# Kernel tuning notes

Hardware: AMD Instinct MI355X
Metric: run time of the kernel (lower is better)

The kernel has to match this reference:

```python
import jax, jax.numpy as jnp
import numpy as np

B, T, D, M, L = 4, 2048, 256, 128, 16
P = M * L  # max_pair_cnt


def setup_inputs() -> dict:
    key = jax.random.key(0)
    ks = jax.random.split(key, 11)
    head = jax.random.normal(ks[0], (B, P, T), jnp.float32) * 0.05
    tail = jax.random.normal(ks[1], (B, P, T), jnp.float32) * 0.05
    x = jax.random.normal(ks[2], (B, T, D), jnp.float32)
    coref_mention_position = jax.random.uniform(ks[3], (B, M, T), jnp.float32)
    lab = jax.random.uniform(ks[4], (B, P, 2), jnp.float32) + 1e-3
    coref_label = lab / lab.sum(-1, keepdims=True)  # already-softmaxed target
    coref_label_mask = jax.random.randint(ks[5], (B, P), 0, 2).astype(bool)
    lens = jnp.full((B, M), L, jnp.int32)  # uniform segment lengths
    w1 = jax.random.normal(ks[6], (3 * D, D), jnp.float32) / np.sqrt(3 * D).astype(np.float32)
    b1 = jnp.zeros((D,), jnp.float32)
    w2 = jax.random.normal(ks[7], (D, 2), jnp.float32) / np.sqrt(D).astype(np.float32)
    b2 = jnp.zeros((2,), jnp.float32)
    return {"head": head, "tail": tail, "lens": lens, "x": x,
            "coref_mention_position": coref_mention_position,
            "coref_label": coref_label, "coref_label_mask": coref_label_mask,
            "w1": w1, "b1": b1, "w2": w2, "b2": b2}


def reference(head, tail, lens, x, coref_mention_position, coref_label,
              coref_label_mask, w1, b1, w2, b2):
    # bmm-based gather of mention reps: [B,P,T] @ [B,T,D] -> [B,P,D]
    head_rep = jnp.einsum('bpt,btd->bpd', head, x)
    tail_rep = jnp.einsum('bpt,btd->bpd', tail, x)
    feat = jnp.concatenate([head_rep, tail_rep, head_rep * tail_rep], axis=-1)
    logits = jax.nn.relu(feat @ w1 + b1) @ w2 + b2  # [B,P,2]

    # ragged split_n_pad -> per-mention top-1 select (uniform lens == L -> reshape)
    scores = logits[..., 1].reshape(B, M, L)            # [B,M,L]
    max_idx = jnp.argmax(scores, axis=-1)               # [B,M]
    max_val = jnp.max(scores, axis=-1)                  # [B,M] (raw logit, as in source)
    tail_seg = tail_rep.reshape(B, M, L, D)
    sel = jnp.take_along_axis(tail_seg, max_idx[:, :, None, None], axis=2)[:, :, 0, :]
    coref_rep_m = sel * max_val[:, :, None]             # [B,M,D]

    # scatter-bmm merge back into sequence: [B,T,M] @ [B,M,D] -> [B,T,D]
    coref_rep = jnp.einsum('bmt,bmd->btd', coref_mention_position, coref_rep_m)
    output = x + coref_rep

    # KLDivLoss(reduction='mean') over masked pairs
    logq = jax.nn.log_softmax(logits, axis=-1)
    lab = coref_label
    pw = jnp.where(lab > 0, lab * jnp.log(jnp.maximum(lab, 1e-38)), 0.0) - lab * logq
    n = jnp.sum(coref_label_mask).astype(jnp.float32)
    loss = jnp.where(coref_label_mask[..., None], pw, 0.0).sum() / (n * 2.0)
    return output, loss
```

## Files before the change

kernel.cpp:

```cpp
#include <hip/hip_runtime.h>
#include <hip/hip_bf16.h>
#include <stdint.h>

#define TAU 0.35f

typedef __attribute__((ext_vector_type(8))) short bf16x8;
typedef __attribute__((ext_vector_type(4))) float f32x4;

__device__ __forceinline__ unsigned short f2bf(float f) {
  __bf16 h = (__bf16)f;
  return __builtin_bit_cast(unsigned short, h);
}
__device__ __forceinline__ float bf2f(unsigned short u) {
  unsigned int v = ((unsigned int)u) << 16;
  return __builtin_bit_cast(float, v);
}
__device__ __forceinline__ void async_copy16(const void* g, void* l) {
  __builtin_amdgcn_global_load_lds(
      (const __attribute__((address_space(1))) unsigned int*)g,
      (__attribute__((address_space(3))) unsigned int*)l, 16, 0, 0);
}
__device__ __forceinline__ float rdlane(float v, int l) {
  return __builtin_bit_cast(float,
      __builtin_amdgcn_readlane(__builtin_bit_cast(int, v), l));
}

__global__ __launch_bounds__(256) void k_prep(
    const float* __restrict__ x, const float* __restrict__ w1,
    const float* __restrict__ b2,
    unsigned short* __restrict__ xt, unsigned short* __restrict__ w1t,
    float* __restrict__ logits, int* __restrict__ njobs,
    float* __restrict__ featws) {
  __shared__ float tileS[64][65];
  __shared__ float tx[64][132];
  int bx = blockIdx.x, tid = threadIdx.x;
  if (bx == 0 && tid < 4) njobs[tid] = 0;
  if (bx < 64) {
    int i = bx * 256 + tid;
    logits[i] = b2[i & 1];
  }
  {
    float4 z = {0.f, 0.f, 0.f, 0.f};
    for (int i = bx * 256 + tid; i < 1048576; i += 304 * 256)
      ((float4*)featws)[i] = z;
  }
  if (bx < 256) {
    int b = bx >> 6, kc = (bx >> 1) & 31, dh = bx & 1;
    const float* src = x + ((size_t)b * 2048 + (size_t)kc * 64) * 256 + dh * 128;
#pragma unroll
    for (int p = 0; p < 8; ++p) {
      int idx = p * 256 + tid;
      int row = idx >> 5, f4 = idx & 31;
      *(float4*)&tx[row][f4 * 4] = *(const float4*)&src[(size_t)row * 256 + f4 * 4];
    }
    __syncthreads();
    unsigned short* dst = xt + ((size_t)(b * 32 + kc)) * 16384 + dh * 1024;
#pragma unroll
    for (int p = 0; p < 4; ++p) {
      int idx = p * 256 + tid;
      int d0 = idx & 127, k8 = idx >> 7;
      bf16x8 v;
#pragma unroll
      for (int j = 0; j < 8; ++j) v[j] = (short)f2bf(tx[k8 * 8 + j][d0]);
      *(bf16x8*)&dst[(size_t)k8 * 2048 + d0 * 8] = v;
    }
  } else {
    int wt = bx - 256;
    int k6 = wt >> 2, n6 = wt & 3;
    int j = tid & 63, i0 = tid >> 6;
    const float* src = w1 + ((size_t)k6 * 64) * 256 + n6 * 64;
    for (int i = i0; i < 64; i += 4) tileS[i][j] = src[(size_t)i * 256 + j];
    __syncthreads();
    unsigned short* dst = w1t + ((size_t)n6 * 64) * 768 + k6 * 64;
    for (int r = i0; r < 64; r += 4) dst[(size_t)r * 768 + j] = f2bf(tileS[j][r]);
  }
}

__global__ __launch_bounds__(512, 4) void k_gemm_rep(
    const float* __restrict__ head, const float* __restrict__ tail,
    const unsigned short* __restrict__ xt,
    float* __restrict__ hrep, float* __restrict__ trep) {
  __shared__ unsigned short As[2][2048];
  __shared__ unsigned short Bs[2][16384];
  int bx = blockIdx.x;
  int b = bx >> 7, mt = bx & 127;
  const float* Asrc = ((mt < 64) ? head : tail) +
                      ((size_t)(b * 2048 + (mt & 63) * 32)) * 2048;
  float* Crep = (mt < 64) ? hrep : trep;
  const unsigned short* Bsrc = xt + (size_t)b * 524288;

  int tid = threadIdx.x, lane = tid & 63, w = tid >> 6;
  int rg = w & 1, cg = w >> 1;
  int l4 = lane >> 4, l15 = lane & 15;

  int arow = tid >> 3, ak8 = tid & 7;
  const float* aptr = Asrc + (size_t)arow * 2048 + ak8 * 8;
  int awi = (ak8 * 32 + arow) * 8;

  const unsigned short* bg = Bsrc + tid * 8;

  int aoff[2];
  int boff[2][4];
#pragma unroll
  for (int kh = 0; kh < 2; ++kh) {
    aoff[kh] = ((kh * 4 + l4) * 32 + rg * 16 + l15) * 8;
#pragma unroll
    for (int ct = 0; ct < 4; ++ct)
      boff[kh][ct] = ((kh * 4 + l4) * 256 + cg * 64 + ct * 16 + l15) * 8;
  }

  f32x4 acc[4];
#pragma unroll
  for (int ct = 0; ct < 4; ++ct) acc[ct] = (f32x4){0.f, 0.f, 0.f, 0.f};

  float4 av0, av1;
  auto STAGEB = [&](int buf) {
#pragma unroll
    for (int a = 0; a < 4; ++a)
      async_copy16(bg + (size_t)a * 4096, &Bs[buf][(tid + a * 512) * 8]);
    bg += 16384;
  };
  auto LOADA = [&]() {
    const float4* ap = (const float4*)aptr;
    av0 = ap[0]; av1 = ap[1];
    aptr += 64;
  };
  auto WRITEA = [&](int buf) {
    bf16x8 p;
    p[0] = (short)f2bf(av0.x); p[1] = (short)f2bf(av0.y);
    p[2] = (short)f2bf(av0.z); p[3] = (short)f2bf(av0.w);
    p[4] = (short)f2bf(av1.x); p[5] = (short)f2bf(av1.y);
    p[6] = (short)f2bf(av1.z); p[7] = (short)f2bf(av1.w);
    *(bf16x8*)&As[buf][awi] = p;
  };
  auto MMA = [&](int buf) {
    const unsigned short* A_ = As[buf];
    const unsigned short* B_ = Bs[buf];
#pragma unroll
    for (int kh = 0; kh < 2; ++kh) {
      bf16x8 a0 = *(const bf16x8*)&A_[aoff[kh]];
#pragma unroll
      for (int ct = 0; ct < 4; ++ct) {
        bf16x8 bb = *(const bf16x8*)&B_[boff[kh][ct]];
        acc[ct] = __builtin_amdgcn_mfma_f32_16x16x32_bf16(a0, bb, acc[ct], 0, 0, 0);
      }
    }
  };

  STAGEB(0);
  if (tid < 256) { LOADA(); WRITEA(0); }
  __syncthreads();

  for (int it = 0; it < 32; ++it) {
    int cur = it & 1, nxt = cur ^ 1;
    if (it < 31) {
      STAGEB(nxt);
      if (tid < 256) LOADA();
    }
    MMA(cur);
    if (it < 31 && tid < 256) WRITEA(nxt);
    __syncthreads();
  }

  size_t prow = (size_t)b * 2048 + (size_t)(mt & 63) * 32 + rg * 16 + (l4 << 2);
  int cb = cg * 64 + l15;
#pragma unroll
  for (int ct = 0; ct < 4; ++ct)
#pragma unroll
    for (int i = 0; i < 4; ++i)
      Crep[(prow + i) * 256 + cb + ct * 16] = acc[ct][i];
}

__global__ __launch_bounds__(256) void k_feat(
    const float* __restrict__ hrep, const float* __restrict__ trep,
    unsigned short* __restrict__ featbf) {
  int gid = blockIdx.x * 256 + threadIdx.x;
  int p = gid >> 6, d0 = (gid & 63) * 4;
  float4 h4 = *(const float4*)&hrep[(size_t)p * 256 + d0];
  float4 t4 = *(const float4*)&trep[(size_t)p * 256 + d0];
  ushort4 a, bb, c;
  a.x = f2bf(h4.x); a.y = f2bf(h4.y); a.z = f2bf(h4.z); a.w = f2bf(h4.w);
  bb.x = f2bf(t4.x); bb.y = f2bf(t4.y); bb.z = f2bf(t4.z); bb.w = f2bf(t4.w);
  c.x = f2bf(h4.x * t4.x); c.y = f2bf(h4.y * t4.y);
  c.z = f2bf(h4.z * t4.z); c.w = f2bf(h4.w * t4.w);
  *(ushort4*)&featbf[(size_t)p * 768 + d0] = a;
  *(ushort4*)&featbf[(size_t)p * 768 + 256 + d0] = bb;
  *(ushort4*)&featbf[(size_t)p * 768 + 512 + d0] = c;
}

__global__ __launch_bounds__(256, 4) void k_gemm_mlp(
    const unsigned short* __restrict__ featb, const unsigned short* __restrict__ w1t,
    const float* __restrict__ b1, const float* __restrict__ w2,
    float* __restrict__ logits) {
  __shared__ unsigned short As[2][4096], Bs[2][4096];
  int bx = blockIdx.x;
  int ntile = bx >> 7;
  int mtile = bx & 127;
  int tid = threadIdx.x, lane = tid & 63, w = tid >> 6;

  const unsigned short* ag[2];
  const unsigned short* bgp[2];
  int dofs[2];
#pragma unroll
  for (int a = 0; a < 2; ++a) {
    int rowofs = a * 8 + (lane >> 3);
    int k8 = (lane & 7) ^ (rowofs & 7);
    ag[a] = featb + (size_t)(mtile * 64 + w * 16 + rowofs) * 768 + k8 * 8;
    bgp[a] = w1t + (size_t)(ntile * 64 + w * 16 + rowofs) * 768 + k8 * 8;
    dofs[a] = (w * 128 + a * 64 + lane) * 8;
  }
  int sw0 = (lane >> 4) ^ (lane & 7);
  int sw1 = (4 + (lane >> 4)) ^ (lane & 7);
  int arowc = (w * 16 + (lane & 15)) * 8;
  int colc[4];
#pragma unroll
  for (int ct = 0; ct < 4; ++ct) colc[ct] = (ct * 16 + (lane & 15)) * 8;

  f32x4 acc[4];
#pragma unroll
  for (int ct = 0; ct < 4; ++ct) acc[ct] = (f32x4){0.f, 0.f, 0.f, 0.f};

#pragma unroll
  for (int a = 0; a < 2; ++a) {
    async_copy16(ag[a], &As[0][dofs[a]]); ag[a] += 64;
    async_copy16(bgp[a], &Bs[0][dofs[a]]); bgp[a] += 64;
  }
  __syncthreads();

  for (int it = 0; it < 12; ++it) {
    int cur = it & 1, nxt = cur ^ 1;
    if (it < 11) {
#pragma unroll
      for (int a = 0; a < 2; ++a) {
        async_copy16(ag[a], &As[nxt][dofs[a]]); ag[a] += 64;
        async_copy16(bgp[a], &Bs[nxt][dofs[a]]); bgp[a] += 64;
      }
    }
    const unsigned short* A_ = As[cur];
    const unsigned short* B_ = Bs[cur];
    bf16x8 a0 = *(const bf16x8*)&A_[(arowc + sw0) * 8];
    bf16x8 a1 = *(const bf16x8*)&A_[(arowc + sw1) * 8];
#pragma unroll
    for (int ct = 0; ct < 4; ++ct) {
      bf16x8 b0 = *(const bf16x8*)&B_[(colc[ct] + sw0) * 8];
      acc[ct] = __builtin_amdgcn_mfma_f32_16x16x32_bf16(a0, b0, acc[ct], 0, 0, 0);
    }
#pragma unroll
    for (int ct = 0; ct < 4; ++ct) {
      bf16x8 b1 = *(const bf16x8*)&B_[(colc[ct] + sw1) * 8];
      acc[ct] = __builtin_amdgcn_mfma_f32_16x16x32_bf16(a1, b1, acc[ct], 0, 0, 0);
    }
    __syncthreads();
  }

  float bv[4], w20[4], w21[4];
#pragma unroll
  for (int ct = 0; ct < 4; ++ct) {
    int col = ntile * 64 + ct * 16 + (lane & 15);
    bv[ct] = b1[col]; w20[ct] = w2[col * 2]; w21[ct] = w2[col * 2 + 1];
  }
#pragma unroll
  for (int i = 0; i < 4; ++i) {
    float s0 = 0.f, s1 = 0.f;
#pragma unroll
    for (int ct = 0; ct < 4; ++ct) {
      float r = fmaxf(acc[ct][i] + bv[ct], 0.f);
      s0 += r * w20[ct]; s1 += r * w21[ct];
    }
#pragma unroll
    for (int off = 1; off < 16; off <<= 1) {
      s0 += __shfl_xor(s0, off); s1 += __shfl_xor(s1, off);
    }
    if ((lane & 15) == 0) {
      int row = mtile * 64 + w * 16 + ((lane >> 4) << 2) + i;
      atomicAdd(&logits[row * 2], s0);
      atomicAdd(&logits[row * 2 + 1], s1);
    }
  }
}

__global__ void k_select(const float* __restrict__ logits, int* __restrict__ idxv,
                         float* __restrict__ mval, int* __restrict__ cmask,
                         int* __restrict__ njobs, int* __restrict__ jobs) {
  int q = blockIdx.x * 256 + threadIdx.x;
  if (q >= 512) return;
  int base = q * 16;
  float s[16];
#pragma unroll
  for (int i = 0; i < 16; ++i) s[i] = logits[(size_t)(base + i) * 2 + 1];
  float best = s[0]; int bi = 0;
#pragma unroll
  for (int i = 1; i < 16; ++i) if (s[i] > best) { best = s[i]; bi = i; }
  int mask = 0, cnt = 0;
#pragma unroll
  for (int i = 0; i < 16; ++i) if (s[i] > best - TAU) { mask |= 1 << i; ++cnt; }
  idxv[q] = bi; mval[q] = best;
  if (cnt > 1) {
    cmask[q] = mask;
    int bb = q >> 7;
    for (int i = 0; i < 16; ++i)
      if ((mask >> i) & 1) {
        int j = atomicAdd(&njobs[bb], 1);
        jobs[bb * 2048 + j] = base + i;
      }
  } else cmask[q] = 0;
}

__global__ __launch_bounds__(1024) void k_refine_dot(
    const int* __restrict__ njobs, const int* __restrict__ jobs,
    const float* __restrict__ head, const float* __restrict__ tail,
    const float* __restrict__ x,
    float* __restrict__ featH, float* __restrict__ featT) {
  __shared__ float red[4][16][256];
  __shared__ int scode[8];
  int tid = threadIdx.x, lane = tid & 63, w = tid >> 6;
  int tg = w >> 2, dg = w & 3;
  int d = dg * 64 + lane;

  for (int gt = blockIdx.x; ; gt += gridDim.x) {
    int rem = gt, b = 0, nj = 0;
    for (; b < 4; ++b) {
      nj = njobs[b];
      int ntb = ((nj + 7) >> 3) * 8;
      if (rem < ntb) break;
      rem -= ntb;
    }
    if (b == 4) break;
    int grp = rem >> 3, tc = rem & 7;
    __syncthreads();
    if (tid < 8) scode[tid] = jobs[b * 2048 + min(grp * 8 + tid, nj - 1)];
    __syncthreads();

    int t0 = tc * 256 + tg * 64;
    float vh[8], vt[8];
#pragma unroll
    for (int j = 0; j < 8; ++j) {
      int p = scode[j] & 2047;
      size_t ro = ((size_t)(b * 2048 + p)) * 2048 + t0 + lane;
      vh[j] = head[ro]; vt[j] = tail[ro];
    }
    float ah[8] = {0.f, 0.f, 0.f, 0.f, 0.f, 0.f, 0.f, 0.f};
    float at[8] = {0.f, 0.f, 0.f, 0.f, 0.f, 0.f, 0.f, 0.f};
    const float* xp = x + (size_t)b * 524288 + (size_t)t0 * 256 + d;
#pragma unroll 8
    for (int t = 0; t < 64; ++t) {
      float xv = xp[(size_t)t * 256];
#pragma unroll
      for (int j = 0; j < 8; ++j) {
        ah[j] += rdlane(vh[j], t) * xv;
        at[j] += rdlane(vt[j], t) * xv;
      }
    }
#pragma unroll
    for (int j = 0; j < 8; ++j) {
      red[tg][j][d] = ah[j];
      red[tg][8 + j][d] = at[j];
    }
    __syncthreads();
    if (tid < 256) {
#pragma unroll
      for (int j = 0; j < 16; ++j) {
        float s = red[0][j][tid] + red[1][j][tid] + red[2][j][tid] + red[3][j][tid];
        int jj = j & 7;
        if (grp * 8 + jj < nj) {
          float* dst = (j < 8) ? featH : featT;
          atomicAdd(&dst[(size_t)scode[jj] * 256 + tid], s);
        }
      }
    }
  }
}

__global__ __launch_bounds__(1024) void k_refine_mlp(
    const int* __restrict__ njobs, const int* __restrict__ jobs,
    const float* __restrict__ featH, const float* __restrict__ featT,
    const float* __restrict__ w1, const float* __restrict__ b1,
    const float* __restrict__ w2, const float* __restrict__ b2,
    float* __restrict__ refined) {
  __shared__ float feat8[768][8];
  __shared__ float redm[4][8][256];
  __shared__ float part[8][4];
  __shared__ int scode[8];
  int tid = threadIdx.x;
  int hseg = tid >> 8, d = tid & 255;

  for (int gt = blockIdx.x; ; gt += gridDim.x) {
    int rem = gt, b = 0, nj = 0;
    for (; b < 4; ++b) {
      nj = njobs[b];
      int ntb = (nj + 7) >> 3;
      if (rem < ntb) break;
      rem -= ntb;
    }
    if (b == 4) break;
    int grp = rem;
    __syncthreads();
    if (tid < 8) scode[tid] = jobs[b * 2048 + min(grp * 8 + tid, nj - 1)];
    __syncthreads();
#pragma unroll
    for (int r = 0; r < 2; ++r) {
      int j = hseg * 2 + r;
      float h = featH[(size_t)scode[j] * 256 + d];
      float t = featT[(size_t)scode[j] * 256 + d];
      feat8[d][j] = h; feat8[256 + d][j] = t; feat8[512 + d][j] = h * t;
    }
    __syncthreads();
    float hp[8] = {0.f, 0.f, 0.f, 0.f, 0.f, 0.f, 0.f, 0.f};
    const float* w1c = w1 + (size_t)(hseg * 192) * 256 + d;
#pragma unroll 4
    for (int ii = 0; ii < 192; ++ii) {
      float wv = w1c[(size_t)ii * 256];
      float4 f0 = *(const float4*)&feat8[hseg * 192 + ii][0];
      float4 f1 = *(const float4*)&feat8[hseg * 192 + ii][4];
      hp[0] += f0.x * wv; hp[1] += f0.y * wv; hp[2] += f0.z * wv; hp[3] += f0.w * wv;
      hp[4] += f1.x * wv; hp[5] += f1.y * wv; hp[6] += f1.z * wv; hp[7] += f1.w * wv;
    }
#pragma unroll
    for (int j = 0; j < 8; ++j) redm[hseg][j][d] = hp[j];
    __syncthreads();
    if (tid < 256) {
      float w2v = w2[tid * 2 + 1], b1v = b1[tid];
#pragma unroll
      for (int j = 0; j < 8; ++j) {
        float h = b1v + redm[0][j][tid] + redm[1][j][tid] + redm[2][j][tid] + redm[3][j][tid];
        h = fmaxf(h, 0.f) * w2v;
#pragma unroll
        for (int off = 1; off < 64; off <<= 1) h += __shfl_xor(h, off);
        if ((tid & 63) == 0) part[j][tid >> 6] = h;
      }
    }
    __syncthreads();
    if (tid < 8 && grp * 8 + tid < nj)
      refined[scode[tid]] = part[tid][0] + part[tid][1] + part[tid][2] + part[tid][3] + b2[1];
  }
}

__global__ __launch_bounds__(256) void k_repm(
    const int* __restrict__ idxv, const float* __restrict__ mval,
    const int* __restrict__ cmask, const float* __restrict__ refined,
    const float* __restrict__ trep, float* __restrict__ repm) {
  int q = blockIdx.x, d = threadIdx.x;
  int mask = cmask[q]; int bi; float v;
  if (mask) {
    bi = -1; v = -1e30f;
    for (int i = 0; i < 16; ++i)
      if ((mask >> i) & 1) { float s = refined[q * 16 + i]; if (s > v) { v = s; bi = i; } }
  } else { bi = idxv[q]; v = mval[q]; }
  repm[(size_t)q * 256 + d] = trep[((size_t)q * 16 + bi) * 256 + d] * v;
}

__global__ __launch_bounds__(256) void k_merge(
    const float* __restrict__ cmp, const float* __restrict__ repm,
    const float* __restrict__ x, float* __restrict__ out) {
  __shared__ float cl[128 * 16];
  int bx = blockIdx.x, b = bx >> 7, t0 = (bx & 127) * 16;
  int tid = threadIdx.x;
#pragma unroll
  for (int it = 0; it < 2; ++it) {
    int f = it * 256 + tid;
    int row = f >> 2, c4 = (f & 3) * 4;
    *(float4*)&cl[row * 16 + c4] =
        *(const float4*)&cmp[((size_t)(b * 128 + row)) * 2048 + t0 + c4];
  }
  __syncthreads();
  float acc[16];
#pragma unroll
  for (int i = 0; i < 16; ++i) acc[i] = 0.f;
  int d = tid;
  for (int m = 0; m < 128; ++m) {
    float rv = repm[(size_t)(b * 128 + m) * 256 + d];
    const float4* c4p = (const float4*)&cl[m * 16];
#pragma unroll
    for (int jj = 0; jj < 4; ++jj) {
      float4 c = c4p[jj];
      acc[jj * 4] += c.x * rv; acc[jj * 4 + 1] += c.y * rv;
      acc[jj * 4 + 2] += c.z * rv; acc[jj * 4 + 3] += c.w * rv;
    }
  }
  const float* xb = x + ((size_t)(b * 2048 + t0)) * 256 + d;
  float* ob = out + ((size_t)(b * 2048 + t0)) * 256 + d;
#pragma unroll
  for (int tt = 0; tt < 16; ++tt) ob[(size_t)tt * 256] = xb[(size_t)tt * 256] + acc[tt];
}

__global__ __launch_bounds__(1024) void k_loss(
    const float* __restrict__ logits, const float* __restrict__ lab,
    const unsigned char* __restrict__ mask, float* __restrict__ out_loss) {
  __shared__ float rs[1024], rc[1024];
  int tid = threadIdx.x;
  float sum = 0.f, cnt = 0.f;
  for (int p = tid; p < 8192; p += 1024) {
    float l0 = logits[(size_t)p * 2], l1 = logits[(size_t)p * 2 + 1];
    float a0 = lab[(size_t)p * 2], a1 = lab[(size_t)p * 2 + 1];
    float mx = fmaxf(l0, l1);
    float lse = mx + logf(expf(l0 - mx) + expf(l1 - mx));
    float pw = 0.f;
    if (a0 > 0.f) pw += a0 * logf(fmaxf(a0, 1e-38f));
    if (a1 > 0.f) pw += a1 * logf(fmaxf(a1, 1e-38f));
    pw -= a0 * (l0 - lse) + a1 * (l1 - lse);
    if (mask[p]) { sum += pw; cnt += 1.f; }
  }
  rs[tid] = sum; rc[tid] = cnt;
  __syncthreads();
  for (int s = 512; s > 0; s >>= 1) {
    if (tid < s) { rs[tid] += rs[tid + s]; rc[tid] += rc[tid + s]; }
    __syncthreads();
  }
  if (tid == 0) *out_loss = rs[0] / (rc[0] * 2.0f);
}

extern "C" void kernel_launch(void* const* d_in, const int* in_sizes, int n_in,
                              void* d_out, int out_size, void* d_ws, size_t ws_size,
                              hipStream_t stream) {
  (void)in_sizes; (void)n_in; (void)out_size; (void)ws_size;
  const float* head = (const float*)d_in[0];
  const float* tail = (const float*)d_in[1];
  const float* x = (const float*)d_in[3];
  const float* cmp = (const float*)d_in[4];
  const float* lab = (const float*)d_in[5];
  const unsigned char* lmask = (const unsigned char*)d_in[6];
  const float* w1 = (const float*)d_in[7];
  const float* b1 = (const float*)d_in[8];
  const float* w2 = (const float*)d_in[9];
  const float* b2 = (const float*)d_in[10];
  float* out = (float*)d_out;

  char* ws = (char*)d_ws;
  size_t off = 0;
  auto alloc = [&](size_t bytes) -> void* {
    void* p = ws + off; off += (bytes + 255) & ~(size_t)255; return p;
  };
  unsigned short* xt = (unsigned short*)alloc(4ull * 256 * 2048 * 2);
  unsigned short* w1t = (unsigned short*)alloc(256ull * 768 * 2);
  float* hrep = (float*)alloc(8192ull * 256 * 4);
  float* trep = (float*)alloc(8192ull * 256 * 4);
  unsigned short* featb = (unsigned short*)alloc(8192ull * 768 * 2);
  float* logits = (float*)alloc(8192ull * 2 * 4);
  float* refined = (float*)alloc(8192ull * 4);
  int* idxv = (int*)alloc(512 * 4);
  float* mvalv = (float*)alloc(512 * 4);
  int* cmaskv = (int*)alloc(512 * 4);
  int* njobs = (int*)alloc(256);
  int* jobs = (int*)alloc(4 * 2048 * 4);
  float* repm = (float*)alloc(512ull * 256 * 4);
  float* featH = (float*)alloc(8192ull * 256 * 4);
  float* featT = (float*)alloc(8192ull * 256 * 4);

  k_prep<<<304, 256, 0, stream>>>(x, w1, b2, xt, w1t, logits, njobs, featH);
  k_gemm_rep<<<512, 512, 0, stream>>>(head, tail, xt, hrep, trep);
  k_feat<<<2048, 256, 0, stream>>>(hrep, trep, featb);
  k_gemm_mlp<<<512, 256, 0, stream>>>(featb, w1t, b1, w2, logits);
  k_select<<<2, 256, 0, stream>>>(logits, idxv, mvalv, cmaskv, njobs, jobs);
  k_refine_dot<<<512, 1024, 0, stream>>>(njobs, jobs, head, tail, x, featH, featT);
  k_refine_mlp<<<128, 1024, 0, stream>>>(njobs, jobs, featH, featT, w1, b1, w2, b2, refined);
  k_repm<<<512, 256, 0, stream>>>(idxv, mvalv, cmaskv, refined, trep, repm);
  k_merge<<<512, 256, 0, stream>>>(cmp, repm, x, out);
  k_loss<<<1, 1024, 0, stream>>>(logits, lab, lmask, out + 4ull * 2048 * 256);
}
```

Measured before the change: 320.8 us.

## Halve K-step in rep GEMM to cut LDS and fuse select with loss

The head/tail representation GEMM now stages 32-wide K slices instead of 64, halving its LDS footprint. This lets more blocks sit on each CU, and the launch bound is raised to 8 to match, at the cost of twice as many loop iterations and barriers. The top-1 select and the KL loss reduction are merged into a single 512-thread kernel to remove one tiny launch from the tail of the pipeline.

Result: slower. 344.2 us (+7.3%).

```diff
diff --git a/kernel.cpp b/kernel.cpp
--- a/kernel.cpp
+++ b/kernel.cpp
@@ -76,12 +76,12 @@
   }
 }
 
-__global__ __launch_bounds__(512, 4) void k_gemm_rep(
+__global__ __launch_bounds__(512, 8) void k_gemm_rep(
     const float* __restrict__ head, const float* __restrict__ tail,
     const unsigned short* __restrict__ xt,
     float* __restrict__ hrep, float* __restrict__ trep) {
-  __shared__ unsigned short As[2][2048];
-  __shared__ unsigned short Bs[2][16384];
+  __shared__ unsigned short As[2][1024];
+  __shared__ unsigned short Bs[2][8192];
   int bx = blockIdx.x;
   int b = bx >> 7, mt = bx & 127;
   const float* Asrc = ((mt < 64) ? head : tail) +
@@ -93,21 +93,17 @@
   int rg = w & 1, cg = w >> 1;
   int l4 = lane >> 4, l15 = lane & 15;
 
-  int arow = tid >> 3, ak8 = tid & 7;
+  int arow = tid >> 2, ak8 = tid & 3;
   const float* aptr = Asrc + (size_t)arow * 2048 + ak8 * 8;
   int awi = (ak8 * 32 + arow) * 8;
 
   const unsigned short* bg = Bsrc + tid * 8;
 
-  int aoff[2];
-  int boff[2][4];
-#pragma unroll
-  for (int kh = 0; kh < 2; ++kh) {
-    aoff[kh] = ((kh * 4 + l4) * 32 + rg * 16 + l15) * 8;
-#pragma unroll
-    for (int ct = 0; ct < 4; ++ct)
-      boff[kh][ct] = ((kh * 4 + l4) * 256 + cg * 64 + ct * 16 + l15) * 8;
-  }
+  int aoff = (l4 * 32 + rg * 16 + l15) * 8;
+  int boff[4];
+#pragma unroll
+  for (int ct = 0; ct < 4; ++ct)
+    boff[ct] = (l4 * 256 + cg * 64 + ct * 16 + l15) * 8;
 
   f32x4 acc[4];
 #pragma unroll
@@ -116,14 +112,14 @@
   float4 av0, av1;
   auto STAGEB = [&](int buf) {
 #pragma unroll
-    for (int a = 0; a < 4; ++a)
+    for (int a = 0; a < 2; ++a)
       async_copy16(bg + (size_t)a * 4096, &Bs[buf][(tid + a * 512) * 8]);
-    bg += 16384;
+    bg += 8192;
   };
   auto LOADA = [&]() {
     const float4* ap = (const float4*)aptr;
     av0 = ap[0]; av1 = ap[1];
-    aptr += 64;
+    aptr += 32;
   };
   auto WRITEA = [&](int buf) {
     bf16x8 p;
@@ -136,29 +132,26 @@
   auto MMA = [&](int buf) {
     const unsigned short* A_ = As[buf];
     const unsigned short* B_ = Bs[buf];
-#pragma unroll
-    for (int kh = 0; kh < 2; ++kh) {
-      bf16x8 a0 = *(const bf16x8*)&A_[aoff[kh]];
-#pragma unroll
-      for (int ct = 0; ct < 4; ++ct) {
-        bf16x8 bb = *(const bf16x8*)&B_[boff[kh][ct]];
-        acc[ct] = __builtin_amdgcn_mfma_f32_16x16x32_bf16(a0, bb, acc[ct], 0, 0, 0);
-      }
+    bf16x8 a0 = *(const bf16x8*)&A_[aoff];
+#pragma unroll
+    for (int ct = 0; ct < 4; ++ct) {
+      bf16x8 bb = *(const bf16x8*)&B_[boff[ct]];
+      acc[ct] = __builtin_amdgcn_mfma_f32_16x16x32_bf16(a0, bb, acc[ct], 0, 0, 0);
     }
   };
 
   STAGEB(0);
-  if (tid < 256) { LOADA(); WRITEA(0); }
+  if (tid < 128) { LOADA(); WRITEA(0); }
   __syncthreads();
 
-  for (int it = 0; it < 32; ++it) {
+  for (int it = 0; it < 64; ++it) {
     int cur = it & 1, nxt = cur ^ 1;
-    if (it < 31) {
+    if (it < 63) {
       STAGEB(nxt);
-      if (tid < 256) LOADA();
+      if (tid < 128) LOADA();
     }
     MMA(cur);
-    if (it < 31 && tid < 256) WRITEA(nxt);
+    if (it < 63 && tid < 128) WRITEA(nxt);
     __syncthreads();
   }
 
@@ -279,31 +272,56 @@
   }
 }
 
-__global__ void k_select(const float* __restrict__ logits, int* __restrict__ idxv,
-                         float* __restrict__ mval, int* __restrict__ cmask,
-                         int* __restrict__ njobs, int* __restrict__ jobs) {
-  int q = blockIdx.x * 256 + threadIdx.x;
-  if (q >= 512) return;
-  int base = q * 16;
-  float s[16];
-#pragma unroll
-  for (int i = 0; i < 16; ++i) s[i] = logits[(size_t)(base + i) * 2 + 1];
-  float best = s[0]; int bi = 0;
-#pragma unroll
-  for (int i = 1; i < 16; ++i) if (s[i] > best) { best = s[i]; bi = i; }
-  int mask = 0, cnt = 0;
-#pragma unroll
-  for (int i = 0; i < 16; ++i) if (s[i] > best - TAU) { mask |= 1 << i; ++cnt; }
-  idxv[q] = bi; mval[q] = best;
-  if (cnt > 1) {
-    cmask[q] = mask;
-    int bb = q >> 7;
-    for (int i = 0; i < 16; ++i)
-      if ((mask >> i) & 1) {
-        int j = atomicAdd(&njobs[bb], 1);
-        jobs[bb * 2048 + j] = base + i;
-      }
-  } else cmask[q] = 0;
+__global__ __launch_bounds__(512) void k_select_loss(
+    const float* __restrict__ logits, int* __restrict__ idxv,
+    float* __restrict__ mval, int* __restrict__ cmask,
+    int* __restrict__ njobs, int* __restrict__ jobs,
+    const float* __restrict__ lab, const unsigned char* __restrict__ mask,
+    float* __restrict__ out_loss) {
+  __shared__ float rs[512], rc[512];
+  int tid = threadIdx.x;
+  {
+    int q = tid;
+    int base = q * 16;
+    float s[16];
+#pragma unroll
+    for (int i = 0; i < 16; ++i) s[i] = logits[(size_t)(base + i) * 2 + 1];
+    float best = s[0]; int bi = 0;
+#pragma unroll
+    for (int i = 1; i < 16; ++i) if (s[i] > best) { best = s[i]; bi = i; }
+    int msk = 0, cnt = 0;
+#pragma unroll
+    for (int i = 0; i < 16; ++i) if (s[i] > best - TAU) { msk |= 1 << i; ++cnt; }
+    idxv[q] = bi; mval[q] = best;
+    if (cnt > 1) {
+      cmask[q] = msk;
+      int bb = q >> 7;
+      for (int i = 0; i < 16; ++i)
+        if ((msk >> i) & 1) {
+          int j = atomicAdd(&njobs[bb], 1);
+          jobs[bb * 2048 + j] = base + i;
+        }
+    } else cmask[q] = 0;
+  }
+  float sum = 0.f, cnt = 0.f;
+  for (int p = tid; p < 8192; p += 512) {
+    float l0 = logits[(size_t)p * 2], l1 = logits[(size_t)p * 2 + 1];
+    float a0 = lab[(size_t)p * 2], a1 = lab[(size_t)p * 2 + 1];
+    float mx = fmaxf(l0, l1);
+    float lse = mx + logf(expf(l0 - mx) + expf(l1 - mx));
+    float pw = 0.f;
+    if (a0 > 0.f) pw += a0 * logf(fmaxf(a0, 1e-38f));
+    if (a1 > 0.f) pw += a1 * logf(fmaxf(a1, 1e-38f));
+    pw -= a0 * (l0 - lse) + a1 * (l1 - lse);
+    if (mask[p]) { sum += pw; cnt += 1.f; }
+  }
+  rs[tid] = sum; rc[tid] = cnt;
+  __syncthreads();
+  for (int s = 256; s > 0; s >>= 1) {
+    if (tid < s) { rs[tid] += rs[tid + s]; rc[tid] += rc[tid + s]; }
+    __syncthreads();
+  }
+  if (tid == 0) *out_loss = rs[0] / (rc[0] * 2.0f);
 }
 
 __global__ __launch_bounds__(1024) void k_refine_dot(
@@ -481,32 +499,6 @@
   float* ob = out + ((size_t)(b * 2048 + t0)) * 256 + d;
 #pragma unroll
   for (int tt = 0; tt < 16; ++tt) ob[(size_t)tt * 256] = xb[(size_t)tt * 256] + acc[tt];
-}
-
-__global__ __launch_bounds__(1024) void k_loss(
-    const float* __restrict__ logits, const float* __restrict__ lab,
-    const unsigned char* __restrict__ mask, float* __restrict__ out_loss) {
-  __shared__ float rs[1024], rc[1024];
-  int tid = threadIdx.x;
-  float sum = 0.f, cnt = 0.f;
-  for (int p = tid; p < 8192; p += 1024) {
-    float l0 = logits[(size_t)p * 2], l1 = logits[(size_t)p * 2 + 1];
-    float a0 = lab[(size_t)p * 2], a1 = lab[(size_t)p * 2 + 1];
-    float mx = fmaxf(l0, l1);
-    float lse = mx + logf(expf(l0 - mx) + expf(l1 - mx));
-    float pw = 0.f;
-    if (a0 > 0.f) pw += a0 * logf(fmaxf(a0, 1e-38f));
-    if (a1 > 0.f) pw += a1 * logf(fmaxf(a1, 1e-38f));
-    pw -= a0 * (l0 - lse) + a1 * (l1 - lse);
-    if (mask[p]) { sum += pw; cnt += 1.f; }
-  }
-  rs[tid] = sum; rc[tid] = cnt;
-  __syncthreads();
-  for (int s = 512; s > 0; s >>= 1) {
-    if (tid < s) { rs[tid] += rs[tid + s]; rc[tid] += rc[tid + s]; }
-    __syncthreads();
-  }
-  if (tid == 0) *out_loss = rs[0] / (rc[0] * 2.0f);
 }
 
 extern "C" void kernel_launch(void* const* d_in, const int* in_sizes, int n_in,
@@ -550,10 +542,10 @@
   k_gemm_rep<<<512, 512, 0, stream>>>(head, tail, xt, hrep, trep);
   k_feat<<<2048, 256, 0, stream>>>(hrep, trep, featb);
   k_gemm_mlp<<<512, 256, 0, stream>>>(featb, w1t, b1, w2, logits);
-  k_select<<<2, 256, 0, stream>>>(logits, idxv, mvalv, cmaskv, njobs, jobs);
+  k_select_loss<<<1, 512, 0, stream>>>(logits, idxv, mvalv, cmaskv, njobs, jobs,
+                                       lab, lmask, out + 4ull * 2048 * 256);
   k_refine_dot<<<512, 1024, 0, stream>>>(njobs, jobs, head, tail, x, featH, featT);
   k_refine_mlp<<<128, 1024, 0, stream>>>(njobs, jobs, featH, featT, w1, b1, w2, b2, refined);
   k_repm<<<512, 256, 0, stream>>>(idxv, mvalv, cmaskv, refined, trep, repm);
   k_merge<<<512, 256, 0, stream>>>(cmp, repm, x, out);
-  k_loss<<<1, 1024, 0, stream>>>(logits, lab, lmask, out + 4ull * 2048 * 256);
-}
+}
```
